# Performance work log

Measured on AMD Instinct MI355X. Metric: run time of the kernel, lower is better.

The kernel has to match this reference:

```python
import jax, jax.numpy as jnp
import numpy as np

HIDDEN = 1024
HEADS = 16
HEAD_DIM = HIDDEN // HEADS
EPS = 1e-5


def setup_inputs() -> dict:
    key = jax.random.key(0)
    ks = jax.random.split(key, 8)
    B, S, D = 2, 2048, HIDDEN
    s = 1.0 / np.sqrt(D)
    return {
        "x": jax.random.normal(ks[0], (B, S, D), dtype=jnp.float32),
        "Wq": jax.random.uniform(ks[1], (D, D), jnp.float32, -s, s),
        "bq": jnp.zeros((D,), jnp.float32),
        "Wk": jax.random.uniform(ks[2], (D, D), jnp.float32, -s, s),
        "bk": jnp.zeros((D,), jnp.float32),
        "Wv": jax.random.uniform(ks[3], (D, D), jnp.float32, -s, s),
        "bv": jnp.zeros((D,), jnp.float32),
        "gamma": jnp.ones((D,), jnp.float32),
        "beta": jnp.zeros((D,), jnp.float32),
    }


def reference(x, Wq, bq, Wk, bk, Wv, bv, gamma, beta):
    B, S, D = x.shape
    H, Hd = HEADS, HEAD_DIM
    # QKV projections -> [B, H, S, Hd]
    q = (x @ Wq + bq).reshape(B, S, H, Hd).transpose(0, 2, 1, 3)
    k = (x @ Wk + bk).reshape(B, S, H, Hd).transpose(0, 2, 1, 3)
    v = (x @ Wv + bv).reshape(B, S, H, Hd).transpose(0, 2, 1, 3)
    scores = jnp.einsum('bhqd,bhkd->bhqk', q, k) / np.sqrt(Hd).astype(np.float32)
    attn = jax.nn.softmax(scores, axis=-1)  # dropout identity in eval
    ctx = jnp.einsum('bhqk,bhkd->bhqd', attn, v)
    ctx = ctx.transpose(0, 2, 1, 3).reshape(B, S, D)
    y = x + ctx
    mu = jnp.mean(y, axis=-1, keepdims=True)
    var = jnp.var(y, axis=-1, keepdims=True)
    out = (y - mu) * jax.lax.rsqrt(var + EPS) * gamma + beta
    return out, attn.mean(axis=1)
```

## Files before the change

kernel.cpp:

```cpp
#include <hip/hip_runtime.h>

#define S_LEN 2048
#define DIM   1024
#define NH    16
#define HD    64

typedef __bf16 bf16x8 __attribute__((ext_vector_type(8)));
typedef __bf16 bf16x4 __attribute__((ext_vector_type(4)));
typedef float  f32x4  __attribute__((ext_vector_type(4)));
typedef float  f32x16 __attribute__((ext_vector_type(16)));
typedef unsigned int u32x4 __attribute__((ext_vector_type(4)));

#define SCALE_Q (0.125f * 1.44269504088896f)

#define GLOAD_LDS16(g, l) __builtin_amdgcn_global_load_lds( \
    (const __attribute__((address_space(1))) void*)(g),     \
    (__attribute__((address_space(3))) void*)(l), 16, 0, 0)

static __device__ __forceinline__ unsigned cvt_pk_bf16(float a, float b) {
  unsigned r;
  asm("v_cvt_pk_bf16_f32 %0, %1, %2" : "=v"(r) : "v"(a), "v"(b));
  return r;
}

__global__ __launch_bounds__(256) void cast_x_kernel(const float* __restrict__ x,
                                                     __bf16* __restrict__ xb) {
  int i = blockIdx.x * 256 + threadIdx.x;
  const float4 a = ((const float4*)x)[i * 2];
  const float4 b = ((const float4*)x)[i * 2 + 1];
  bf16x8 o;
  o[0] = (__bf16)a.x; o[1] = (__bf16)a.y; o[2] = (__bf16)a.z; o[3] = (__bf16)a.w;
  o[4] = (__bf16)b.x; o[5] = (__bf16)b.y; o[6] = (__bf16)b.z; o[7] = (__bf16)b.w;
  ((bf16x8*)xb)[i] = o;
}

__global__ __launch_bounds__(256) void transW_kernel(const float* __restrict__ Wq,
                                                     const float* __restrict__ Wk,
                                                     const float* __restrict__ Wv,
                                                     __bf16* __restrict__ WT) {
  int which = blockIdx.z;
  const float* W = (which == 0) ? Wq : ((which == 1) ? Wk : Wv);
  __bf16* o = WT + (size_t)which * DIM * DIM;
  __shared__ __bf16 t[64][65];
  int k0 = blockIdx.y * 64, n0 = blockIdx.x * 64;
  int tid = threadIdx.x;
  int c4 = (tid & 15) * 4, rb = tid >> 4;
#pragma unroll
  for (int p = 0; p < 4; ++p) {
    int r = p * 16 + rb;
    float4 a = *(const float4*)&W[(size_t)(k0 + r) * DIM + n0 + c4];
    t[r][c4 + 0] = (__bf16)a.x; t[r][c4 + 1] = (__bf16)a.y;
    t[r][c4 + 2] = (__bf16)a.z; t[r][c4 + 3] = (__bf16)a.w;
  }
  __syncthreads();
#pragma unroll
  for (int p = 0; p < 4; ++p) {
    int n = p * 16 + rb;
    bf16x4 v;
    v[0] = t[c4 + 0][n]; v[1] = t[c4 + 1][n];
    v[2] = t[c4 + 2][n]; v[3] = t[c4 + 3][n];
    *(bf16x4*)&o[(size_t)(n0 + n) * DIM + k0 + c4] = v;
  }
}

__global__ __launch_bounds__(256) void qkv_gemm_kernel(const __bf16* __restrict__ xb,
                                                       const __bf16* __restrict__ WT,
                                                       const float* __restrict__ bq,
                                                       const float* __restrict__ bk,
                                                       const float* __restrict__ bv,
                                                       __bf16* __restrict__ qkv) {
  int which = blockIdx.z;
  const __bf16* Wt = WT + (size_t)which * DIM * DIM;
  const float* bias = (which == 0) ? bq : ((which == 1) ? bk : bv);
  __bf16* outp = qkv + (size_t)which * 2 * NH * S_LEN * HD;
  int m0 = blockIdx.y * 128;
  int n0 = blockIdx.x * 128;
  __shared__ __align__(16) char smem[36864];
  __bf16 (*As)[64] = (__bf16(*)[64])smem;
  __bf16 (*Bs)[64] = (__bf16(*)[64])(smem + 16384);
  __bf16 (*Ct)[136] = (__bf16(*)[136])smem;
  int tid = threadIdx.x;
  int wave = tid >> 6, lane = tid & 63;
  int g = lane >> 4, l15 = lane & 15;
  int wm = (wave >> 1) * 64, wn = (wave & 1) * 64;
  int lr = lane >> 3;
  int lc = (lane & 7) * 8;
  const __bf16* ga = &xb[(size_t)(m0 + wave * 32 + lr) * DIM + lc];
  const __bf16* gb = &Wt[(size_t)(n0 + wave * 32 + lr) * DIM + lc];
  f32x4 acc[4][4] = {};
  for (int k0 = 0; k0 < DIM; k0 += 64) {
#pragma unroll
    for (int c = 0; c < 4; ++c) {
      GLOAD_LDS16(ga + k0 + (size_t)(c * 8) * DIM, &As[wave * 32 + c * 8][0]);
      GLOAD_LDS16(gb + k0 + (size_t)(c * 8) * DIM, &Bs[wave * 32 + c * 8][0]);
    }
    __syncthreads();
#pragma unroll
    for (int ks = 0; ks < 2; ++ks) {
      bf16x8 af[4], bfr[4];
#pragma unroll
      for (int s = 0; s < 4; ++s) {
        af[s]  = *(const bf16x8*)&As[wm + s * 16 + l15][ks * 32 + g * 8];
        bfr[s] = *(const bf16x8*)&Bs[wn + s * 16 + l15][ks * 32 + g * 8];
      }
#pragma unroll
      for (int i = 0; i < 4; ++i)
#pragma unroll
        for (int j = 0; j < 4; ++j)
          acc[i][j] = __builtin_amdgcn_mfma_f32_16x16x32_bf16(af[i], bfr[j], acc[i][j], 0, 0, 0);
    }
    __syncthreads();
  }
  if (which != 2) {
    float scale = (which == 0) ? SCALE_Q : 1.0f;
#pragma unroll
    for (int i = 0; i < 4; ++i)
#pragma unroll
      for (int j = 0; j < 4; ++j) {
        int n = n0 + wn + j * 16 + l15;
        float bval = bias[n];
#pragma unroll
        for (int r = 0; r < 4; ++r) {
          int m = m0 + wm + i * 16 + g * 4 + r;
          float val = (acc[i][j][r] + bval) * scale;
          int bb = m >> 11, ss = m & 2047;
          int hh = n >> 6, hd = n & 63;
          outp[(((size_t)bb * NH + hh) * S_LEN + ss) * HD + hd] = (__bf16)val;
        }
      }
  } else {
#pragma unroll
    for (int i = 0; i < 4; ++i)
#pragma unroll
      for (int j = 0; j < 4; ++j) {
        int nl = wn + j * 16 + l15;
        float bval = bias[n0 + nl];
        bf16x4 t;
#pragma unroll
        for (int r = 0; r < 4; ++r) t[r] = (__bf16)(acc[i][j][r] + bval);
        *(bf16x4*)&Ct[nl][wm + i * 16 + g * 4] = t;
      }
    __syncthreads();
#pragma unroll
    for (int it = 0; it < 8; ++it) {
      int idx = (it * 256 + tid) * 8;
      int row = idx >> 7, col = idx & 127;
      int n = n0 + row, hh = n >> 6, hd = n & 63;
      int m = m0 + col, bb = m >> 11, ss = m & 2047;
      *(bf16x8*)&outp[(((size_t)bb * NH + hh) * HD + hd) * S_LEN + ss] =
          *(const bf16x8*)&Ct[row][col];
    }
  }
}

__global__ __launch_bounds__(512, 4) void attn_flash_kernel(const __bf16* __restrict__ qw,
                                                            const __bf16* __restrict__ kw,
                                                            const __bf16* __restrict__ vtw,
                                                            const float* __restrict__ x,
                                                            float* __restrict__ y,
                                                            float* __restrict__ c_out) {
  int qt = blockIdx.x;
  int h  = blockIdx.y;
  int b  = blockIdx.z;
  size_t hoff = (size_t)(b * NH + h) * S_LEN * HD;
  const __bf16* qh = qw + hoff;
  const __bf16* kh = kw + hoff;
  const __bf16* vth = vtw + hoff;
  __shared__ __align__(16) char smem[33792];
  __bf16 (*Ks)[64] = (__bf16(*)[64])smem;
  __bf16 (*Vt)[64] = (__bf16(*)[64])(smem + 16384);
  float (*ctxbuf)[64] = (float(*)[64])smem;
  float* mlbuf = (float*)(smem + 32768);
  int tid = threadIdx.x;
  int wave = tid >> 6, lane = tid & 63;
  int half = wave >> 2, wsub = wave & 3;
  int l31 = lane & 31, hi = lane >> 5;
  int swz = (l31 & 7) << 3;
  int q = qt * 128 + wsub * 32 + l31;
  int qlocal = wsub * 32 + l31;
  __bf16 (*Ksh)[64] = Ks + half * 64;
  __bf16 (*Vth)[64] = Vt + half * 64;
  bf16x8 qf[4];
#pragma unroll
  for (int ks = 0; ks < 4; ++ks)
    qf[ks] = *(const bf16x8*)&qh[(size_t)q * HD + ks * 16 + hi * 8];
  int st = tid & 255;
  int sr0 = st >> 3;
  int sc  = (st & 7) * 8;
  int swzs = (sr0 & 7) << 3;
  int pl = (sc & 8) ? sc - 4 : sc;
  int ph = (sc & 8) ? sc + 4 : sc + 8;
  bf16x8 kv[2], vv[2];
  {
    int kt0 = half;
#pragma unroll
    for (int i = 0; i < 2; ++i) {
      int r = sr0 + i * 32;
      kv[i] = *(const bf16x8*)&kh[(size_t)(kt0 * 64 + r) * HD + sc];
      vv[i] = *(const bf16x8*)&vth[(size_t)r * S_LEN + kt0 * 64 + sc];
    }
  }
  float m_r = -1e30f, l_r = 0.f;
  f32x16 ctx0 = {}, ctx1 = {};
  for (int t = 0; t < 16; ++t) {
    __syncthreads();
#pragma unroll
    for (int i = 0; i < 2; ++i) {
      int r = sr0 + i * 32;
      *(bf16x8*)&Ksh[r][sc ^ swzs] = kv[i];
      bf16x4 vlo, vhi4;
#pragma unroll
      for (int e = 0; e < 4; ++e) { vlo[e] = vv[i][e]; vhi4[e] = vv[i][e + 4]; }
      *(bf16x4*)&Vth[r][pl ^ swzs] = vlo;
      *(bf16x4*)&Vth[r][ph ^ swzs] = vhi4;
    }
    if (t < 15) {
      int ktn = 2 * (t + 1) + half;
#pragma unroll
      for (int i = 0; i < 2; ++i) {
        int r = sr0 + i * 32;
        kv[i] = *(const bf16x8*)&kh[(size_t)(ktn * 64 + r) * HD + sc];
        vv[i] = *(const bf16x8*)&vth[(size_t)r * S_LEN + ktn * 64 + sc];
      }
    }
    __syncthreads();
    f32x16 s0 = {}, s1 = {};
    __builtin_amdgcn_s_setprio(1);
#pragma unroll
    for (int ks = 0; ks < 4; ++ks) {
      bf16x8 k0 = *(const bf16x8*)&Ksh[l31][(ks * 16 + hi * 8) ^ swz];
      bf16x8 k1 = *(const bf16x8*)&Ksh[32 + l31][(ks * 16 + hi * 8) ^ swz];
      s0 = __builtin_amdgcn_mfma_f32_32x32x16_bf16(k0, qf[ks], s0, 0, 0, 0);
      s1 = __builtin_amdgcn_mfma_f32_32x32x16_bf16(k1, qf[ks], s1, 0, 0, 0);
    }
    __builtin_amdgcn_s_setprio(0);
    float vmax = s0[0];
#pragma unroll
    for (int r = 1; r < 16; ++r) vmax = fmaxf(vmax, s0[r]);
#pragma unroll
    for (int r = 0; r < 16; ++r) vmax = fmaxf(vmax, s1[r]);
    vmax = fmaxf(vmax, __shfl_xor(vmax, 32));
    if (__any(vmax > m_r)) {
      float mnew = fmaxf(m_r, vmax);
      float alpha = __builtin_amdgcn_exp2f(m_r - mnew);
      m_r = mnew;
      ctx0 *= alpha; ctx1 *= alpha; l_r *= alpha;
    }
    float ps = 0.f;
#pragma unroll
    for (int r = 0; r < 16; ++r) { s0[r] = __builtin_amdgcn_exp2f(s0[r] - m_r); ps += s0[r]; }
#pragma unroll
    for (int r = 0; r < 16; ++r) { s1[r] = __builtin_amdgcn_exp2f(s1[r] - m_r); ps += s1[r]; }
    ps += __shfl_xor(ps, 32);
    l_r += ps;
    bf16x8 pa[4];
#pragma unroll
    for (int f = 0; f < 2; ++f) {
      u32x4 tt;
#pragma unroll
      for (int j = 0; j < 4; ++j) tt[j] = cvt_pk_bf16(s0[f * 8 + 2 * j], s0[f * 8 + 2 * j + 1]);
      pa[f] = __builtin_bit_cast(bf16x8, tt);
    }
#pragma unroll
    for (int f = 0; f < 2; ++f) {
      u32x4 tt;
#pragma unroll
      for (int j = 0; j < 4; ++j) tt[j] = cvt_pk_bf16(s1[f * 8 + 2 * j], s1[f * 8 + 2 * j + 1]);
      pa[2 + f] = __builtin_bit_cast(bf16x8, tt);
    }
    __builtin_amdgcn_s_setprio(1);
#pragma unroll
    for (int f = 0; f < 4; ++f) {
      bf16x8 v0 = *(const bf16x8*)&Vth[l31][(f * 16 + hi * 8) ^ swz];
      bf16x8 v1 = *(const bf16x8*)&Vth[32 + l31][(f * 16 + hi * 8) ^ swz];
      ctx0 = __builtin_amdgcn_mfma_f32_32x32x16_bf16(v0, pa[f], ctx0, 0, 0, 0);
      ctx1 = __builtin_amdgcn_mfma_f32_32x32x16_bf16(v1, pa[f], ctx1, 0, 0, 0);
    }
    __builtin_amdgcn_s_setprio(0);
  }
  __syncthreads();
  int sw2 = (qlocal & 7) << 2;
  if (half == 1) {
#pragma unroll
    for (int rq = 0; rq < 4; ++rq) {
      int hd0 = rq * 8 + hi * 4;
      f32x4 a, bb;
#pragma unroll
      for (int j = 0; j < 4; ++j) { a[j] = ctx0[rq * 4 + j]; bb[j] = ctx1[rq * 4 + j]; }
      *(f32x4*)&ctxbuf[qlocal][hd0 ^ sw2] = a;
      *(f32x4*)&ctxbuf[qlocal][(32 + hd0) ^ sw2] = bb;
    }
    if (hi == 0) { mlbuf[qlocal] = m_r; mlbuf[128 + qlocal] = l_r; }
  }
  __syncthreads();
  if (half == 0) {
    float m1 = mlbuf[qlocal], l1 = mlbuf[128 + qlocal];
    float m = fmaxf(m_r, m1);
    float a0 = __builtin_amdgcn_exp2f(m_r - m);
    float a1 = __builtin_amdgcn_exp2f(m1 - m);
    float l = a0 * l_r + a1 * l1;
    float il = 1.0f / l;
    float cvl = m + __builtin_amdgcn_logf(l);
    if (lane < 32)
      c_out[(size_t)(b * NH + h) * S_LEN + qt * 128 + wsub * 32 + lane] = cvl;
    size_t ybase = ((size_t)b * S_LEN + q) * DIM + h * HD;
#pragma unroll
    for (int rq = 0; rq < 4; ++rq) {
      int hd0 = rq * 8 + hi * 4;
      f32x4 c1 = *(const f32x4*)&ctxbuf[qlocal][hd0 ^ sw2];
      float4 xv0 = *(const float4*)&x[ybase + hd0];
      float4 o0;
      o0.x = xv0.x + (a0 * ctx0[rq * 4 + 0] + a1 * c1[0]) * il;
      o0.y = xv0.y + (a0 * ctx0[rq * 4 + 1] + a1 * c1[1]) * il;
      o0.z = xv0.z + (a0 * ctx0[rq * 4 + 2] + a1 * c1[2]) * il;
      o0.w = xv0.w + (a0 * ctx0[rq * 4 + 3] + a1 * c1[3]) * il;
      *(float4*)&y[ybase + hd0] = o0;
      int hd1 = 32 + hd0;
      f32x4 c2 = *(const f32x4*)&ctxbuf[qlocal][hd1 ^ sw2];
      float4 xv1 = *(const float4*)&x[ybase + hd1];
      float4 o1;
      o1.x = xv1.x + (a0 * ctx1[rq * 4 + 0] + a1 * c2[0]) * il;
      o1.y = xv1.y + (a0 * ctx1[rq * 4 + 1] + a1 * c2[1]) * il;
      o1.z = xv1.z + (a0 * ctx1[rq * 4 + 2] + a1 * c2[2]) * il;
      o1.w = xv1.w + (a0 * ctx1[rq * 4 + 3] + a1 * c2[3]) * il;
      *(float4*)&y[ybase + hd1] = o1;
    }
  }
}

__global__ __launch_bounds__(256) void attn_mean_kernel(const __bf16* __restrict__ qw,
                                                        const __bf16* __restrict__ kw,
                                                        const float* __restrict__ c_in,
                                                        float* __restrict__ out_mean) {
  int kt = blockIdx.x, qt = blockIdx.y, b = blockIdx.z;
  __shared__ __align__(16) __bf16 Ks[64][64];
  int tid = threadIdx.x;
  int wave = tid >> 6, lane = tid & 63;
  int l31 = lane & 31, hi = lane >> 5;
  int swz = (l31 & 7) << 3;
  int q = qt * 128 + wave * 32 + l31;
  const __bf16* qp = qw + (size_t)b * NH * S_LEN * HD;
  const __bf16* kp = kw + (size_t)b * NH * S_LEN * HD;
  int sr0 = tid >> 3;
  int sc  = (tid & 7) * 8;
  int swzs = (sr0 & 7) << 3;
  bf16x8 kv[2];
#pragma unroll
  for (int i = 0; i < 2; ++i)
    kv[i] = *(const bf16x8*)&kp[(size_t)(kt * 64 + sr0 + i * 32) * HD + sc];
  f32x16 macc0 = {}, macc1 = {};
  for (int h = 0; h < NH; ++h) {
    size_t hb = (size_t)h * S_LEN * HD;
    bf16x8 qfr[4];
#pragma unroll
    for (int ks = 0; ks < 4; ++ks)
      qfr[ks] = *(const bf16x8*)&qp[hb + (size_t)q * HD + ks * 16 + hi * 8];
    __syncthreads();
#pragma unroll
    for (int i = 0; i < 2; ++i)
      *(bf16x8*)&Ks[sr0 + i * 32][sc ^ swzs] = kv[i];
    if (h < NH - 1) {
      size_t hbn = (size_t)(h + 1) * S_LEN * HD;
#pragma unroll
      for (int i = 0; i < 2; ++i)
        kv[i] = *(const bf16x8*)&kp[hbn + (size_t)(kt * 64 + sr0 + i * 32) * HD + sc];
    }
    __syncthreads();
    f32x16 s0 = {}, s1 = {};
    __builtin_amdgcn_s_setprio(1);
#pragma unroll
    for (int ks = 0; ks < 4; ++ks) {
      bf16x8 k0 = *(const bf16x8*)&Ks[l31][(ks * 16 + hi * 8) ^ swz];
      bf16x8 k1 = *(const bf16x8*)&Ks[32 + l31][(ks * 16 + hi * 8) ^ swz];
      s0 = __builtin_amdgcn_mfma_f32_32x32x16_bf16(k0, qfr[ks], s0, 0, 0, 0);
      s1 = __builtin_amdgcn_mfma_f32_32x32x16_bf16(k1, qfr[ks], s1, 0, 0, 0);
    }
    __builtin_amdgcn_s_setprio(0);
    float c = c_in[(size_t)(b * NH + h) * S_LEN + q];
#pragma unroll
    for (int r = 0; r < 16; ++r) macc0[r] += __builtin_amdgcn_exp2f(s0[r] - c);
#pragma unroll
    for (int r = 0; r < 16; ++r) macc1[r] += __builtin_amdgcn_exp2f(s1[r] - c);
  }
  const float invh = 1.0f / (float)NH;
  size_t obase = ((size_t)b * S_LEN + q) * S_LEN + kt * 64;
#pragma unroll
  for (int rq = 0; rq < 4; ++rq) {
    int k0i = rq * 8 + hi * 4;
    float4 o0;
    o0.x = macc0[rq * 4 + 0] * invh; o0.y = macc0[rq * 4 + 1] * invh;
    o0.z = macc0[rq * 4 + 2] * invh; o0.w = macc0[rq * 4 + 3] * invh;
    *(float4*)&out_mean[obase + k0i] = o0;
    float4 o1;
    o1.x = macc1[rq * 4 + 0] * invh; o1.y = macc1[rq * 4 + 1] * invh;
    o1.z = macc1[rq * 4 + 2] * invh; o1.w = macc1[rq * 4 + 3] * invh;
    *(float4*)&out_mean[obase + 32 + k0i] = o1;
  }
}

__global__ __launch_bounds__(256) void ln_kernel(const float* __restrict__ y,
                                                 const float* __restrict__ gamma,
                                                 const float* __restrict__ beta,
                                                 float* __restrict__ out) {
  int row = blockIdx.x;
  const float* yr = y + (size_t)row * DIM;
  int tid = threadIdx.x;
  float4 v = *(const float4*)&yr[tid * 4];
  float s = v.x + v.y + v.z + v.w;
  float sq = v.x * v.x + v.y * v.y + v.z * v.z + v.w * v.w;
#pragma unroll
  for (int off = 1; off < 64; off <<= 1) {
    s += __shfl_xor(s, off);
    sq += __shfl_xor(sq, off);
  }
  __shared__ float red[8];
  int wave = tid >> 6, lane = tid & 63;
  if (lane == 0) { red[wave] = s; red[4 + wave] = sq; }
  __syncthreads();
  s = red[0] + red[1] + red[2] + red[3];
  sq = red[4] + red[5] + red[6] + red[7];
  float mu = s * (1.0f / DIM);
  float var = sq * (1.0f / DIM) - mu * mu;
  float rstd = rsqrtf(var + 1e-5f);
  float* orow = out + (size_t)row * DIM;
  float4 gv = *(const float4*)&gamma[tid * 4];
  float4 bv = *(const float4*)&beta[tid * 4];
  float4 ov;
  ov.x = (v.x - mu) * rstd * gv.x + bv.x;
  ov.y = (v.y - mu) * rstd * gv.y + bv.y;
  ov.z = (v.z - mu) * rstd * gv.z + bv.z;
  ov.w = (v.w - mu) * rstd * gv.w + bv.w;
  *(float4*)&orow[tid * 4] = ov;
}

extern "C" void kernel_launch(void* const* d_in, const int* in_sizes, int n_in,
                              void* d_out, int out_size, void* d_ws, size_t ws_size,
                              hipStream_t stream) {
  const float* x  = (const float*)d_in[0];
  const float* Wq = (const float*)d_in[1];
  const float* bq = (const float*)d_in[2];
  const float* Wk = (const float*)d_in[3];
  const float* bk = (const float*)d_in[4];
  const float* Wv = (const float*)d_in[5];
  const float* bv = (const float*)d_in[6];
  const float* gamma = (const float*)d_in[7];
  const float* beta  = (const float*)d_in[8];
  float* out = (float*)d_out;

  char* ws = (char*)d_ws;
  __bf16* xb   = (__bf16*)ws;
  __bf16* WT   = (__bf16*)(ws + 8388608);
  __bf16* qkv  = (__bf16*)(ws + 14680064);
  float*  y    = (float*)(ws + 39845888);
  float*  c_ws = (float*)(ws + 56623104);

  cast_x_kernel<<<2048, 256, 0, stream>>>(x, xb);
  transW_kernel<<<dim3(16, 16, 3), 256, 0, stream>>>(Wq, Wk, Wv, WT);
  qkv_gemm_kernel<<<dim3(8, 32, 3), 256, 0, stream>>>(xb, WT, bq, bk, bv, qkv);
  attn_flash_kernel<<<dim3(16, 16, 2), 512, 0, stream>>>(qkv, qkv + 4194304, qkv + 8388608,
                                                         x, y, c_ws);
  attn_mean_kernel<<<dim3(32, 16, 2), 256, 0, stream>>>(qkv, qkv + 4194304, c_ws,
                                                        out + 4194304);
  ln_kernel<<<4096, 256, 0, stream>>>(y, gamma, beta, out);
}
```

Baseline: 181.3 us.

## Double-buffer K/V LDS tiles in flash and mean kernels, one barrier per iteration

Both the flash-attention kernel and the attention-mean kernel now keep two LDS buffers for K (and V) tiles. The next tile is written into the alternate buffer after the current compute, so each loop iteration needs one barrier instead of two. The mean kernel also prefetches Q fragments and the softmax normaliser for the next head into registers. The cost is double the LDS footprint (about 66 KB in the flash kernel), which may cut blocks per CU below the launch_bounds target, plus extra register pressure.

Measured after the change: 182.3 us. About the same (+0.6%).

```diff
diff --git a/kernel.cpp b/kernel.cpp
--- a/kernel.cpp
+++ b/kernel.cpp
@@ -166,11 +166,11 @@
   const __bf16* qh = qw + hoff;
   const __bf16* kh = kw + hoff;
   const __bf16* vth = vtw + hoff;
-  __shared__ __align__(16) char smem[33792];
-  __bf16 (*Ks)[64] = (__bf16(*)[64])smem;
-  __bf16 (*Vt)[64] = (__bf16(*)[64])(smem + 16384);
+  __shared__ __align__(16) char smem[66560];
+  __bf16 (*Kbase)[64] = (__bf16(*)[64])smem;
+  __bf16 (*Vbase)[64] = (__bf16(*)[64])(smem + 32768);
   float (*ctxbuf)[64] = (float(*)[64])smem;
-  float* mlbuf = (float*)(smem + 32768);
+  float* mlbuf = (float*)(smem + 65536);
   int tid = threadIdx.x;
   int wave = tid >> 6, lane = tid & 63;
   int half = wave >> 2, wsub = wave & 3;
@@ -178,8 +178,6 @@
   int swz = (l31 & 7) << 3;
   int q = qt * 128 + wsub * 32 + l31;
   int qlocal = wsub * 32 + l31;
-  __bf16 (*Ksh)[64] = Ks + half * 64;
-  __bf16 (*Vth)[64] = Vt + half * 64;
   bf16x8 qf[4];
 #pragma unroll
   for (int ks = 0; ks < 4; ++ks)
@@ -191,45 +189,48 @@
   int pl = (sc & 8) ? sc - 4 : sc;
   int ph = (sc & 8) ? sc + 4 : sc + 8;
   bf16x8 kv[2], vv[2];
+#pragma unroll
+  for (int i = 0; i < 2; ++i) {
+    int r = sr0 + i * 32;
+    kv[i] = *(const bf16x8*)&kh[(size_t)(half * 64 + r) * HD + sc];
+    vv[i] = *(const bf16x8*)&vth[(size_t)r * S_LEN + half * 64 + sc];
+  }
   {
-    int kt0 = half;
+    __bf16 (*Kd)[64] = Kbase + half * 64;
+    __bf16 (*Vd)[64] = Vbase + half * 64;
 #pragma unroll
     for (int i = 0; i < 2; ++i) {
       int r = sr0 + i * 32;
-      kv[i] = *(const bf16x8*)&kh[(size_t)(kt0 * 64 + r) * HD + sc];
-      vv[i] = *(const bf16x8*)&vth[(size_t)r * S_LEN + kt0 * 64 + sc];
+      *(bf16x8*)&Kd[r][sc ^ swzs] = kv[i];
+      bf16x4 vlo, vhi4;
+#pragma unroll
+      for (int e = 0; e < 4; ++e) { vlo[e] = vv[i][e]; vhi4[e] = vv[i][e + 4]; }
+      *(bf16x4*)&Vd[r][pl ^ swzs] = vlo;
+      *(bf16x4*)&Vd[r][ph ^ swzs] = vhi4;
+    }
+  }
+  {
+    int ktn = 2 + half;
+#pragma unroll
+    for (int i = 0; i < 2; ++i) {
+      int r = sr0 + i * 32;
+      kv[i] = *(const bf16x8*)&kh[(size_t)(ktn * 64 + r) * HD + sc];
+      vv[i] = *(const bf16x8*)&vth[(size_t)r * S_LEN + ktn * 64 + sc];
     }
   }
   float m_r = -1e30f, l_r = 0.f;
   f32x16 ctx0 = {}, ctx1 = {};
+  __syncthreads();
   for (int t = 0; t < 16; ++t) {
-    __syncthreads();
-#pragma unroll
-    for (int i = 0; i < 2; ++i) {
-      int r = sr0 + i * 32;
-      *(bf16x8*)&Ksh[r][sc ^ swzs] = kv[i];
-      bf16x4 vlo, vhi4;
-#pragma unroll
-      for (int e = 0; e < 4; ++e) { vlo[e] = vv[i][e]; vhi4[e] = vv[i][e + 4]; }
-      *(bf16x4*)&Vth[r][pl ^ swzs] = vlo;
-      *(bf16x4*)&Vth[r][ph ^ swzs] = vhi4;
-    }
-    if (t < 15) {
-      int ktn = 2 * (t + 1) + half;
-#pragma unroll
-      for (int i = 0; i < 2; ++i) {
-        int r = sr0 + i * 32;
-        kv[i] = *(const bf16x8*)&kh[(size_t)(ktn * 64 + r) * HD + sc];
-        vv[i] = *(const bf16x8*)&vth[(size_t)r * S_LEN + ktn * 64 + sc];
-      }
-    }
-    __syncthreads();
+    int cur = t & 1;
+    const __bf16 (*Kc)[64] = (const __bf16(*)[64])(Kbase + cur * 128 + half * 64);
+    const __bf16 (*Vc)[64] = (const __bf16(*)[64])(Vbase + cur * 128 + half * 64);
     f32x16 s0 = {}, s1 = {};
     __builtin_amdgcn_s_setprio(1);
 #pragma unroll
     for (int ks = 0; ks < 4; ++ks) {
-      bf16x8 k0 = *(const bf16x8*)&Ksh[l31][(ks * 16 + hi * 8) ^ swz];
-      bf16x8 k1 = *(const bf16x8*)&Ksh[32 + l31][(ks * 16 + hi * 8) ^ swz];
+      bf16x8 k0 = *(const bf16x8*)&Kc[l31][(ks * 16 + hi * 8) ^ swz];
+      bf16x8 k1 = *(const bf16x8*)&Kc[32 + l31][(ks * 16 + hi * 8) ^ swz];
       s0 = __builtin_amdgcn_mfma_f32_32x32x16_bf16(k0, qf[ks], s0, 0, 0, 0);
       s1 = __builtin_amdgcn_mfma_f32_32x32x16_bf16(k1, qf[ks], s1, 0, 0, 0);
     }
@@ -271,14 +272,37 @@
     __builtin_amdgcn_s_setprio(1);
 #pragma unroll
     for (int f = 0; f < 4; ++f) {
-      bf16x8 v0 = *(const bf16x8*)&Vth[l31][(f * 16 + hi * 8) ^ swz];
-      bf16x8 v1 = *(const bf16x8*)&Vth[32 + l31][(f * 16 + hi * 8) ^ swz];
+      bf16x8 v0 = *(const bf16x8*)&Vc[l31][(f * 16 + hi * 8) ^ swz];
+      bf16x8 v1 = *(const bf16x8*)&Vc[32 + l31][(f * 16 + hi * 8) ^ swz];
       ctx0 = __builtin_amdgcn_mfma_f32_32x32x16_bf16(v0, pa[f], ctx0, 0, 0, 0);
       ctx1 = __builtin_amdgcn_mfma_f32_32x32x16_bf16(v1, pa[f], ctx1, 0, 0, 0);
     }
     __builtin_amdgcn_s_setprio(0);
-  }
-  __syncthreads();
+    if (t < 15) {
+      __bf16 (*Kd)[64] = Kbase + (cur ^ 1) * 128 + half * 64;
+      __bf16 (*Vd)[64] = Vbase + (cur ^ 1) * 128 + half * 64;
+#pragma unroll
+      for (int i = 0; i < 2; ++i) {
+        int r = sr0 + i * 32;
+        *(bf16x8*)&Kd[r][sc ^ swzs] = kv[i];
+        bf16x4 vlo, vhi4;
+#pragma unroll
+        for (int e = 0; e < 4; ++e) { vlo[e] = vv[i][e]; vhi4[e] = vv[i][e + 4]; }
+        *(bf16x4*)&Vd[r][pl ^ swzs] = vlo;
+        *(bf16x4*)&Vd[r][ph ^ swzs] = vhi4;
+      }
+      if (t < 14) {
+        int ktn = 2 * (t + 2) + half;
+#pragma unroll
+        for (int i = 0; i < 2; ++i) {
+          int r = sr0 + i * 32;
+          kv[i] = *(const bf16x8*)&kh[(size_t)(ktn * 64 + r) * HD + sc];
+          vv[i] = *(const bf16x8*)&vth[(size_t)r * S_LEN + ktn * 64 + sc];
+        }
+      }
+    }
+    __syncthreads();
+  }
   int sw2 = (qlocal & 7) << 2;
   if (half == 1) {
 #pragma unroll
@@ -333,7 +357,7 @@
                                                         const float* __restrict__ c_in,
                                                         float* __restrict__ out_mean) {
   int kt = blockIdx.x, qt = blockIdx.y, b = blockIdx.z;
-  __shared__ __align__(16) __bf16 Ks[64][64];
+  __shared__ __align__(16) __bf16 Ks[2][64][64];
   int tid = threadIdx.x;
   int wave = tid >> 6, lane = tid & 63;
   int l31 = lane & 31, hi = lane >> 5;
@@ -341,6 +365,7 @@
   int q = qt * 128 + wave * 32 + l31;
   const __bf16* qp = qw + (size_t)b * NH * S_LEN * HD;
   const __bf16* kp = kw + (size_t)b * NH * S_LEN * HD;
+  const float*  cp = c_in + (size_t)b * NH * S_LEN + q;
   int sr0 = tid >> 3;
   int sc  = (tid & 7) * 8;
   int swzs = (sr0 & 7) << 3;
@@ -348,39 +373,59 @@
 #pragma unroll
   for (int i = 0; i < 2; ++i)
     kv[i] = *(const bf16x8*)&kp[(size_t)(kt * 64 + sr0 + i * 32) * HD + sc];
+#pragma unroll
+  for (int i = 0; i < 2; ++i)
+    *(bf16x8*)&Ks[0][sr0 + i * 32][sc ^ swzs] = kv[i];
+#pragma unroll
+  for (int i = 0; i < 2; ++i)
+    kv[i] = *(const bf16x8*)&kp[S_LEN * HD + (size_t)(kt * 64 + sr0 + i * 32) * HD + sc];
+  bf16x8 qc[4], qn[4];
+#pragma unroll
+  for (int ks = 0; ks < 4; ++ks) {
+    qc[ks] = *(const bf16x8*)&qp[(size_t)q * HD + ks * 16 + hi * 8];
+    qn[ks] = *(const bf16x8*)&qp[(size_t)S_LEN * HD + (size_t)q * HD + ks * 16 + hi * 8];
+  }
+  float c_c = cp[0], c_n = cp[S_LEN];
   f32x16 macc0 = {}, macc1 = {};
+  __syncthreads();
   for (int h = 0; h < NH; ++h) {
-    size_t hb = (size_t)h * S_LEN * HD;
-    bf16x8 qfr[4];
-#pragma unroll
-    for (int ks = 0; ks < 4; ++ks)
-      qfr[ks] = *(const bf16x8*)&qp[hb + (size_t)q * HD + ks * 16 + hi * 8];
-    __syncthreads();
-#pragma unroll
-    for (int i = 0; i < 2; ++i)
-      *(bf16x8*)&Ks[sr0 + i * 32][sc ^ swzs] = kv[i];
-    if (h < NH - 1) {
-      size_t hbn = (size_t)(h + 1) * S_LEN * HD;
-#pragma unroll
-      for (int i = 0; i < 2; ++i)
-        kv[i] = *(const bf16x8*)&kp[hbn + (size_t)(kt * 64 + sr0 + i * 32) * HD + sc];
-    }
-    __syncthreads();
+    int cur = h & 1;
     f32x16 s0 = {}, s1 = {};
     __builtin_amdgcn_s_setprio(1);
 #pragma unroll
     for (int ks = 0; ks < 4; ++ks) {
-      bf16x8 k0 = *(const bf16x8*)&Ks[l31][(ks * 16 + hi * 8) ^ swz];
-      bf16x8 k1 = *(const bf16x8*)&Ks[32 + l31][(ks * 16 + hi * 8) ^ swz];
-      s0 = __builtin_amdgcn_mfma_f32_32x32x16_bf16(k0, qfr[ks], s0, 0, 0, 0);
-      s1 = __builtin_amdgcn_mfma_f32_32x32x16_bf16(k1, qfr[ks], s1, 0, 0, 0);
+      bf16x8 k0 = *(const bf16x8*)&Ks[cur][l31][(ks * 16 + hi * 8) ^ swz];
+      bf16x8 k1 = *(const bf16x8*)&Ks[cur][32 + l31][(ks * 16 + hi * 8) ^ swz];
+      s0 = __builtin_amdgcn_mfma_f32_32x32x16_bf16(k0, qc[ks], s0, 0, 0, 0);
+      s1 = __builtin_amdgcn_mfma_f32_32x32x16_bf16(k1, qc[ks], s1, 0, 0, 0);
     }
     __builtin_amdgcn_s_setprio(0);
-    float c = c_in[(size_t)(b * NH + h) * S_LEN + q];
-#pragma unroll
-    for (int r = 0; r < 16; ++r) macc0[r] += __builtin_amdgcn_exp2f(s0[r] - c);
-#pragma unroll
-    for (int r = 0; r < 16; ++r) macc1[r] += __builtin_amdgcn_exp2f(s1[r] - c);
+    if (h < NH - 1) {
+#pragma unroll
+      for (int i = 0; i < 2; ++i)
+        *(bf16x8*)&Ks[cur ^ 1][sr0 + i * 32][sc ^ swzs] = kv[i];
+      if (h < NH - 2) {
+        size_t hbn = (size_t)(h + 2) * S_LEN * HD;
+#pragma unroll
+        for (int i = 0; i < 2; ++i)
+          kv[i] = *(const bf16x8*)&kp[hbn + (size_t)(kt * 64 + sr0 + i * 32) * HD + sc];
+      }
+    }
+#pragma unroll
+    for (int r = 0; r < 16; ++r) macc0[r] += __builtin_amdgcn_exp2f(s0[r] - c_c);
+#pragma unroll
+    for (int r = 0; r < 16; ++r) macc1[r] += __builtin_amdgcn_exp2f(s1[r] - c_c);
+#pragma unroll
+    for (int ks = 0; ks < 4; ++ks) qc[ks] = qn[ks];
+    c_c = c_n;
+    if (h < NH - 2) {
+      size_t hbn = (size_t)(h + 2) * S_LEN * HD;
+#pragma unroll
+      for (int ks = 0; ks < 4; ++ks)
+        qn[ks] = *(const bf16x8*)&qp[hbn + (size_t)q * HD + ks * 16 + hi * 8];
+      c_n = cp[(size_t)(h + 2) * S_LEN];
+    }
+    __syncthreads();
   }
   const float invh = 1.0f / (float)NH;
   size_t obase = ((size_t)b * S_LEN + q) * S_LEN + kt * 64;
```
